# Optimization experiments

Hardware: AMD Instinct MI355X
Metric: run time of the kernel (lower is better)

Reference implementation:

```python
import jax, jax.numpy as jnp
import numpy as np

MAX_LEN = 431
H = 128
B = 2048


def setup_inputs() -> dict:
    key = jax.random.key(0)
    k1, k2, k3, k4, k5 = jax.random.split(key, 5)
    hidden = jax.random.normal(k1, (1, B, H), dtype=jnp.float32)
    k_embedding = jax.random.normal(k2, (MAX_LEN, B, H), dtype=jnp.float32)
    # nn.Linear(2H, H): weight [H, 2H], bias [H]; v: [1, H]
    attn_w = jax.random.normal(k3, (H, 2 * H), dtype=jnp.float32) * (1.0 / np.sqrt(2 * H))
    attn_b = jax.random.normal(k4, (H,), dtype=jnp.float32) * 0.01
    v = jax.random.normal(k5, (1, H), dtype=jnp.float32)
    return {"hidden": hidden, "k_embedding": k_embedding,
            "attn_w": attn_w, "attn_b": attn_b, "v": v}


def reference(hidden, k_embedding, attn_w, attn_b, v):
    # hidden: [1, B, H], k_embedding: [L, B, H]
    # score(b, i) = v . (W @ concat(hidden[:,b], k[i,b]) + bias)
    # Split W over the concat: W1 acts on hidden, W2 on k_embedding.
    h = hidden[0]                      # [B, H]
    w1 = attn_w[:, :H]                 # [H, H]
    w2 = attn_w[:, H:]                 # [H, H]
    # energy[l, b, e] = sum_h h[b,h]*w1[e,h] + sum_h k[l,b,h]*w2[e,h] + b[e]
    energy = (jnp.einsum('bh,eh->be', h, w1)[None, :, :]
              + jnp.einsum('lbh,eh->lbe', k_embedding, w2)
              + attn_b)                # [L, B, H]
    scores = jnp.einsum('lbe,e->lb', energy, v[0])  # [L, B]
    return scores.T                    # [B, L] == attn_energies
```

## Files before the change

### kernel.cpp

```cpp
#include <hip/hip_runtime.h>

#define H 128
#define MAXLEN 431
#define BB 2048


__device__ __forceinline__ float dot4(float4 a, float4 b) {
    return a.x * b.x + a.y * b.y + a.z * b.z + a.w * b.w;
}

__global__ void prep(const float* __restrict__ attn_w,
                     const float* __restrict__ attn_b,
                     const float* __restrict__ v,
                     const float* __restrict__ hidden,
                     float* __restrict__ ws) {
    __shared__ float u1s[H];
    __shared__ float cs;
    const int t = threadIdx.x;

    if (t < 128) {
        float acc = 0.f;
        for (int e = 0; e < H; ++e) acc += v[e] * attn_w[e * 2 * H + t];
        u1s[t] = acc;
    } else {
        int h = t - 128;
        float acc = 0.f;
        for (int e = 0; e < H; ++e) acc += v[e] * attn_w[e * 2 * H + H + h];
        if (blockIdx.x == 0) ws[h] = acc;
    }
    if (t == 0) {
        float c = 0.f;
        for (int e = 0; e < H; ++e) c += attn_b[e] * v[e];
        cs = c;
    }
    __syncthreads();

    const int b = blockIdx.x * 256 + t;
    const float4* h4  = (const float4*)hidden + b * (H / 4);
    const float4* u14 = (const float4*)u1s;
    float a = 0.f;
    #pragma unroll
    for (int j = 0; j < H / 4; ++j) a += dot4(h4[j], u14[j]);
    ws[384 + b] = a + cs;
}

__global__ void main_scores(const float* __restrict__ k_emb,
                            const float* __restrict__ ws,
                            float* __restrict__ out) {
    const int lane = threadIdx.x & 63;
    const int oct  = lane & 7;
    const int rk   = lane >> 3;

    const float4* u2p = (const float4*)ws + oct * 4;
    const float4 u0 = u2p[0], u1 = u2p[1], u2 = u2p[2], u3 = u2p[3];
    const float* hdot = ws + 384;

    const int wid = blockIdx.x * (blockDim.x >> 6) + (threadIdx.x >> 6);
    const int nw  = gridDim.x * (blockDim.x >> 6);
    const int NP  = MAXLEN * BB / 32;

    for (int p = wid; p < NP; p += nw) {
        const int g0 = p * 2;
        const int rowA0 = g0 * 16 + rk;
        const int bA0 = rowA0 & (BB - 1),        bB0 = (rowA0 + 8) & (BB - 1);
        const int bA1 = (rowA0 + 16) & (BB - 1), bB1 = (rowA0 + 24) & (BB - 1);
        float hA0 = hdot[bA0], hB0 = hdot[bB0];
        float hA1 = hdot[bA1], hB1 = hdot[bB1];

        const float4* base = (const float4*)k_emb + (long long)g0 * 512 + rk * 32 + oct * 4;
        float4 a0 = base[0],   a1 = base[1],   a2 = base[2],   a3 = base[3];
        float4 c0 = base[256], c1 = base[257], c2 = base[258], c3 = base[259];
        float4 d0 = base[512], d1 = base[513], d2 = base[514], d3 = base[515];
        float4 e0 = base[768], e1 = base[769], e2 = base[770], e3 = base[771];

        float pa = dot4(a0,u0) + dot4(a1,u1) + dot4(a2,u2) + dot4(a3,u3);
        float pb = dot4(c0,u0) + dot4(c1,u1) + dot4(c2,u2) + dot4(c3,u3);
        float pc = dot4(d0,u0) + dot4(d1,u1) + dot4(d2,u2) + dot4(d3,u3);
        float pd = dot4(e0,u0) + dot4(e1,u1) + dot4(e2,u2) + dot4(e3,u3);

        #pragma unroll
        for (int off = 1; off <= 4; off <<= 1) {
            pa += __shfl_xor(pa, off);
            pb += __shfl_xor(pb, off);
            pc += __shfl_xor(pc, off);
            pd += __shfl_xor(pd, off);
        }

        if (oct == 0) {
            const int lA0 = rowA0 >> 11;
            const int lB0 = (rowA0 + 8) >> 11;
            const int lA1 = (rowA0 + 16) >> 11;
            const int lB1 = (rowA0 + 24) >> 11;
            out[bA0 * MAXLEN + lA0] = pa + hA0;
            out[bB0 * MAXLEN + lB0] = pb + hB0;
            out[bA1 * MAXLEN + lA1] = pc + hA1;
            out[bB1 * MAXLEN + lB1] = pd + hB1;
        }
    }
}

extern "C" void kernel_launch(void* const* d_in, const int* in_sizes, int n_in,
                              void* d_out, int out_size, void* d_ws, size_t ws_size,
                              hipStream_t stream) {
    const float* hidden = (const float*)d_in[0];
    const float* k_emb  = (const float*)d_in[1];
    const float* attn_w = (const float*)d_in[2];
    const float* attn_b = (const float*)d_in[3];
    const float* v      = (const float*)d_in[4];
    float* out = (float*)d_out;
    float* ws  = (float*)d_ws;

    prep<<<8, 256, 0, stream>>>(attn_w, attn_b, v, hidden, ws);
    main_scores<<<1724, 256, 0, stream>>>(k_emb, ws, out);
}
```

Measured before the change: 602.0 us.

## Fuse prep and score kernels into one, recomputing projections per block

Merges the prep kernel into the main scoring kernel. Each block now recomputes the v·W projections into shared memory, and computes the hidden-dot terms for exactly the batch rows it will process. The grid-stride loop becomes a fixed four-iteration loop, since the grid covers all work exactly. This removes one launch, the inter-kernel dependency and the workspace round trip. In exchange, every block re-reads the full weight matrix and its hidden rows, which adds redundant L2 traffic and a serial prologue before the streaming loads begin.

```diff
diff --git a/kernel.cpp b/kernel.cpp
--- a/kernel.cpp
+++ b/kernel.cpp
@@ -3,30 +3,38 @@
 #define H 128
 #define MAXLEN 431
 #define BB 2048
-
+#define NBLK 1724
+#define NWAVES (NBLK * 4)
+#define NP (MAXLEN * BB / 32)
 
 __device__ __forceinline__ float dot4(float4 a, float4 b) {
     return a.x * b.x + a.y * b.y + a.z * b.z + a.w * b.w;
 }
 
-__global__ void prep(const float* __restrict__ attn_w,
-                     const float* __restrict__ attn_b,
-                     const float* __restrict__ v,
-                     const float* __restrict__ hidden,
-                     float* __restrict__ ws) {
+__global__ __launch_bounds__(256) void fused(const float* __restrict__ k_emb,
+                                             const float* __restrict__ hidden,
+                                             const float* __restrict__ attn_w,
+                                             const float* __restrict__ attn_b,
+                                             const float* __restrict__ v,
+                                             float* __restrict__ out) {
     __shared__ float u1s[H];
+    __shared__ float u2s[H];
+    __shared__ float hd[16][32];
     __shared__ float cs;
+
     const int t = threadIdx.x;
 
     if (t < 128) {
         float acc = 0.f;
+        #pragma unroll 8
         for (int e = 0; e < H; ++e) acc += v[e] * attn_w[e * 2 * H + t];
         u1s[t] = acc;
     } else {
-        int h = t - 128;
+        const int h = t - 128;
         float acc = 0.f;
+        #pragma unroll 8
         for (int e = 0; e < H; ++e) acc += v[e] * attn_w[e * 2 * H + H + h];
-        if (blockIdx.x == 0) ws[h] = acc;
+        u2s[h] = acc;
     }
     if (t == 0) {
         float c = 0.f;
@@ -35,37 +43,43 @@
     }
     __syncthreads();
 
-    const int b = blockIdx.x * 256 + t;
-    const float4* h4  = (const float4*)hidden + b * (H / 4);
-    const float4* u14 = (const float4*)u1s;
-    float a = 0.f;
-    #pragma unroll
-    for (int j = 0; j < H / 4; ++j) a += dot4(h4[j], u14[j]);
-    ws[384 + b] = a + cs;
-}
+    {
+        const float4* u14 = (const float4*)u1s;
+        const float cc = cs;
+        #pragma unroll
+        for (int q = 0; q < 2; ++q) {
+            const int idx = t + q * 256;
+            const int s = idx >> 5, j = idx & 31;
+            const int p = blockIdx.x * 4 + (s >> 2) + NWAVES * (s & 3);
+            const int b = (32 * p + j) & (BB - 1);
+            const float4* h4 = (const float4*)hidden + b * (H / 4);
+            float a = 0.f;
+            #pragma unroll
+            for (int jj = 0; jj < H / 4; ++jj) a += dot4(h4[jj], u14[jj]);
+            hd[s][j] = a + cc;
+        }
+    }
+    __syncthreads();
 
-__global__ void main_scores(const float* __restrict__ k_emb,
-                            const float* __restrict__ ws,
-                            float* __restrict__ out) {
-    const int lane = threadIdx.x & 63;
+    const int lane = t & 63;
     const int oct  = lane & 7;
     const int rk   = lane >> 3;
+    const int w    = t >> 6;
 
-    const float4* u2p = (const float4*)ws + oct * 4;
-    const float4 u0 = u2p[0], u1 = u2p[1], u2 = u2p[2], u3 = u2p[3];
-    const float* hdot = ws + 384;
+    const float4* u2p = (const float4*)u2s + oct * 4;
+    const float4 U0 = u2p[0], U1 = u2p[1], U2 = u2p[2], U3 = u2p[3];
 
-    const int wid = blockIdx.x * (blockDim.x >> 6) + (threadIdx.x >> 6);
-    const int nw  = gridDim.x * (blockDim.x >> 6);
-    const int NP  = MAXLEN * BB / 32;
+    const int wid = blockIdx.x * 4 + w;
 
-    for (int p = wid; p < NP; p += nw) {
+    #pragma unroll 1
+    for (int k = 0; k < 4; ++k) {
+        const int p  = wid + NWAVES * k;
         const int g0 = p * 2;
+        const int s  = w * 4 + k;
         const int rowA0 = g0 * 16 + rk;
-        const int bA0 = rowA0 & (BB - 1),        bB0 = (rowA0 + 8) & (BB - 1);
-        const int bA1 = (rowA0 + 16) & (BB - 1), bB1 = (rowA0 + 24) & (BB - 1);
-        float hA0 = hdot[bA0], hB0 = hdot[bB0];
-        float hA1 = hdot[bA1], hB1 = hdot[bB1];
+
+        float hA0 = hd[s][rk],      hB0 = hd[s][rk + 8];
+        float hA1 = hd[s][rk + 16], hB1 = hd[s][rk + 24];
 
         const float4* base = (const float4*)k_emb + (long long)g0 * 512 + rk * 32 + oct * 4;
         float4 a0 = base[0],   a1 = base[1],   a2 = base[2],   a3 = base[3];
@@ -73,10 +87,10 @@
         float4 d0 = base[512], d1 = base[513], d2 = base[514], d3 = base[515];
         float4 e0 = base[768], e1 = base[769], e2 = base[770], e3 = base[771];
 
-        float pa = dot4(a0,u0) + dot4(a1,u1) + dot4(a2,u2) + dot4(a3,u3);
-        float pb = dot4(c0,u0) + dot4(c1,u1) + dot4(c2,u2) + dot4(c3,u3);
-        float pc = dot4(d0,u0) + dot4(d1,u1) + dot4(d2,u2) + dot4(d3,u3);
-        float pd = dot4(e0,u0) + dot4(e1,u1) + dot4(e2,u2) + dot4(e3,u3);
+        float pa = dot4(a0, U0) + dot4(a1, U1) + dot4(a2, U2) + dot4(a3, U3);
+        float pb = dot4(c0, U0) + dot4(c1, U1) + dot4(c2, U2) + dot4(c3, U3);
+        float pc = dot4(d0, U0) + dot4(d1, U1) + dot4(d2, U2) + dot4(d3, U3);
+        float pd = dot4(e0, U0) + dot4(e1, U1) + dot4(e2, U2) + dot4(e3, U3);
 
         #pragma unroll
         for (int off = 1; off <= 4; off <<= 1) {
@@ -87,14 +101,12 @@
         }
 
         if (oct == 0) {
-            const int lA0 = rowA0 >> 11;
-            const int lB0 = (rowA0 + 8) >> 11;
-            const int lA1 = (rowA0 + 16) >> 11;
-            const int lB1 = (rowA0 + 24) >> 11;
-            out[bA0 * MAXLEN + lA0] = pa + hA0;
-            out[bB0 * MAXLEN + lB0] = pb + hB0;
-            out[bA1 * MAXLEN + lA1] = pc + hA1;
-            out[bB1 * MAXLEN + lB1] = pd + hB1;
+            const int bA0 = rowA0 & (BB - 1),        bB0 = (rowA0 + 8) & (BB - 1);
+            const int bA1 = (rowA0 + 16) & (BB - 1), bB1 = (rowA0 + 24) & (BB - 1);
+            out[bA0 * MAXLEN + (rowA0 >> 11)]        = pa + hA0;
+            out[bB0 * MAXLEN + ((rowA0 + 8) >> 11)]  = pb + hB0;
+            out[bA1 * MAXLEN + ((rowA0 + 16) >> 11)] = pc + hA1;
+            out[bB1 * MAXLEN + ((rowA0 + 24) >> 11)] = pd + hB1;
         }
     }
 }
@@ -108,8 +120,8 @@
     const float* attn_b = (const float*)d_in[3];
     const float* v      = (const float*)d_in[4];
     float* out = (float*)d_out;
-    float* ws  = (float*)d_ws;
+    (void)in_sizes; (void)n_in; (void)out_size;
+    (void)d_ws; (void)ws_size;
 
-    prep<<<8, 256, 0, stream>>>(attn_w, attn_b, v, hidden, ws);
-    main_scores<<<1724, 256, 0, stream>>>(k_emb, ws, out);
+    fused<<<NBLK, 256, 0, stream>>>(k_emb, hidden, attn_w, attn_b, v, out);
 }
```

Result: slower. 647.5 us (+7.6%).
